# Performance work log

Hardware: AMD Instinct MI355X
Metric: run time of the kernel (lower is better)

Reference implementation:

```python
import jax, jax.numpy as jnp
import numpy as np

E = 8        # num_expert
D = 768      # d_model
H = 3072     # expert hidden = 4*d_model
K = 2        # top_k
N = 4096     # tokens
C = 2048


def setup_inputs() -> dict:
    key = jax.random.key(0)
    k0, k1, k2, k3 = jax.random.split(key, 4)
    moe_inp = jax.random.normal(k0, (N, D), dtype=jnp.float32)
    gate_w = jax.random.normal(k1, (D, E), dtype=jnp.float32) / np.sqrt(D).astype(np.float32)
    gate_b = jnp.zeros((E,), dtype=jnp.float32)
    w1 = jax.random.normal(k2, (E, D, H), dtype=jnp.float32) / np.sqrt(D).astype(np.float32)
    b1 = jnp.zeros((E, H), dtype=jnp.float32)
    w2 = jax.random.normal(k3, (E, H, D), dtype=jnp.float32) / np.sqrt(H).astype(np.float32)
    b2 = jnp.zeros((E, D), dtype=jnp.float32)
    return {"moe_inp": moe_inp, "gate_w": gate_w, "gate_b": gate_b,
            "w1": w1, "b1": b1, "w2": w2, "b2": b2}


def reference(moe_inp, gate_w, gate_b, w1, b1, w2, b2):
    # --- NaiveGate: linear scores, top-k experts, softmax over the k scores ---
    logits = moe_inp @ gate_w + gate_b                      # [N, E]
    top_v, top_i = jax.lax.top_k(logits, K)                 # [N, K]
    gate_score = jax.nn.softmax(top_v, axis=-1)             # [N, K]

    # --- scatter tokens to expert-contiguous capacity buffers (MOEScatter) ---
    flat_e = top_i.reshape(-1)                              # [N*K] expert id per slot
    onehot = jax.nn.one_hot(flat_e, E, dtype=jnp.int32)     # [N*K, E]
    # running position of each token inside its expert's buffer
    pos = jnp.sum(jnp.cumsum(onehot, axis=0) * onehot, axis=1) - 1  # [N*K]
    x_rep = jnp.repeat(moe_inp, K, axis=0)                  # [N*K, D]
    xe = jnp.zeros((E, C, D), dtype=moe_inp.dtype).at[flat_e, pos].set(x_rep, mode='drop')

    # --- grouped expert FFN (expert_fn): per-expert batched GEMMs ---
    h = jax.nn.gelu(jnp.einsum('ecd,edh->ech', xe, w1) + b1[:, None, :])
    ye = jnp.einsum('ech,ehd->ecd', h, w2) + b2[:, None, :]  # [E, C, D]

    # --- gather back to token order (MOEGather) and combine with gate scores ---
    y_flat = ye.at[flat_e, pos].get(mode='fill', fill_value=0.0)  # [N*K, D]
    out = jnp.einsum('nkd,nk->nd', y_flat.reshape(N, K, D), gate_score)
    return out
```

## Files before the change

kernel.cpp:

```cpp
#include <hip/hip_runtime.h>
#include <hip/hip_bf16.h>
#include <math.h>

#define NT    4096
#define DM    768
#define HD    3072
#define NE    8
#define CAP   2048
#define SLOTS_MAX 9216

typedef __attribute__((ext_vector_type(8))) short bf16x8;
typedef __attribute__((ext_vector_type(4))) float f32x4;

__device__ __forceinline__ unsigned short f2bf(float f) {
  unsigned int u = __float_as_uint(f);
  unsigned int r = (u + 0x7fffu + ((u >> 16) & 1u)) >> 16;
  return (unsigned short)r;
}

__device__ __forceinline__ void async16(const unsigned short* g, unsigned short* l) {
  __builtin_amdgcn_global_load_lds((const __attribute__((address_space(1))) void*)g,
                                   (__attribute__((address_space(3))) void*)l,
                                   16, 0, 0);
}

__global__ void convert_x_kernel(const float* __restrict__ x,
                                 unsigned short* __restrict__ xb) {
  int i = (blockIdx.x * 256 + threadIdx.x) * 4;
  float4 v = *(const float4*)(x + i);
  uint2 o;
  o.x = (unsigned int)f2bf(v.x) | ((unsigned int)f2bf(v.y) << 16);
  o.y = (unsigned int)f2bf(v.z) | ((unsigned int)f2bf(v.w) << 16);
  *(uint2*)(xb + i) = o;
}

__global__ void transpose_kernel(const float* __restrict__ src,
                                 unsigned short* __restrict__ dst,
                                 int R, int src_stride, int col_off,
                                 size_t src_e_stride, size_t dst_e_stride) {
  __shared__ unsigned short tile[64][34];
  const float* s = src + blockIdx.z * src_e_stride;
  unsigned short* d = dst + blockIdx.z * dst_e_stride;
  const int r0 = blockIdx.y * 32;
  const int c0 = blockIdx.x * 64;
  const int t = threadIdx.x;
#pragma unroll
  for (int i = 0; i < 4; i++) {
    int row = (t >> 5) + i * 8;
    int cu  = t & 31;
    const float2 v = *(const float2*)(s + (size_t)(r0 + row) * src_stride + col_off + c0 + cu * 2);
    tile[cu * 2][row]     = f2bf(v.x);
    tile[cu * 2 + 1][row] = f2bf(v.y);
  }
  __syncthreads();
#pragma unroll
  for (int i = 0; i < 4; i++) {
    int drow = (t >> 4) + i * 16;
    int ru   = t & 15;
    unsigned int v = *(const unsigned int*)&tile[drow][ru * 2];
    *(unsigned int*)(d + (size_t)(c0 + drow) * R + r0 + ru * 2) = v;
  }
}

__global__ void gate_dots_kernel(const float* __restrict__ inp,
                                 const float* __restrict__ gw,
                                 const float* __restrict__ gb,
                                 int2* __restrict__ tope,
                                 float2* __restrict__ tops) {
  const int tok  = blockIdx.x * 4 + (threadIdx.x >> 6);
  const int lane = threadIdx.x & 63;
  const float* x = inp + (size_t)tok * DM;
  float acc[NE];
#pragma unroll
  for (int e = 0; e < NE; e++) acc[e] = 0.f;
  for (int d = lane; d < DM; d += 64) {
    float xv = x[d];
    const float4 w0 = *(const float4*)(gw + d * NE);
    const float4 w1v = *(const float4*)(gw + d * NE + 4);
    acc[0] += xv * w0.x; acc[1] += xv * w0.y;
    acc[2] += xv * w0.z; acc[3] += xv * w0.w;
    acc[4] += xv * w1v.x; acc[5] += xv * w1v.y;
    acc[6] += xv * w1v.z; acc[7] += xv * w1v.w;
  }
#pragma unroll
  for (int e = 0; e < NE; e++) {
    float v = acc[e];
#pragma unroll
    for (int m = 32; m > 0; m >>= 1) v += __shfl_xor(v, m, 64);
    acc[e] = v + gb[e];
  }
  if (lane == 0) {
    float bv = -1e30f, sv = -1e30f; int bi = 0, si = 0;
#pragma unroll
    for (int e = 0; e < NE; e++) {
      float v = acc[e];
      if (v > bv)      { sv = bv; si = bi; bv = v; bi = e; }
      else if (v > sv) { sv = v;  si = e; }
    }
    float e1 = expf(sv - bv);
    float s0 = 1.f / (1.f + e1);
    float s1 = e1 / (1.f + e1);
    tope[tok] = make_int2(bi, si);
    tops[tok] = make_float2(s0, s1);
  }
}

__device__ __forceinline__ int agg_inc(int* lcnt, int key) {
  const int lane = threadIdx.x & 63;
  int p = 0;
#pragma unroll
  for (int ee = 0; ee < NE; ee++) {
    unsigned long long m = __ballot(key == ee);
    if (m) {
      int leader = __ffsll(m) - 1;
      int n = __popcll(m);
      int b = 0;
      if (lane == leader) b = atomicAdd(&lcnt[ee], n);
      b = __shfl(b, leader, 64);
      if (key == ee) p = b + __popcll(m & ((1ull << lane) - 1ull));
    }
  }
  return p;
}

__global__ void assign_kernel(const int2* __restrict__ tope,
                              int* __restrict__ cnt,
                              int* __restrict__ base,
                              int* __restrict__ src,
                              int2* __restrict__ pos) {
  __shared__ int lcnt[NE];
  const int t = threadIdx.x;
  if (t < NE) lcnt[t] = 0;
  __syncthreads();
  for (int i = t; i < NT; i += 1024) {
    int2 e = tope[i];
    int p0 = agg_inc(lcnt, e.x);
    int p1 = agg_inc(lcnt, e.y);
    if (p0 < CAP) src[e.x * CAP + p0] = i;
    if (p1 < CAP) src[e.y * CAP + p1] = i;
    pos[i] = make_int2(p0, p1);
  }
  __syncthreads();
  if (t == 0) {
    int b = 0;
    for (int e = 0; e < NE; e++) {
      int c = min(lcnt[e], CAP);
      cnt[e] = c;
      base[e] = b;
      b += (c + 127) & ~127;
    }
  }
}

__global__ __launch_bounds__(256) void gemm1_kernel(
    const unsigned short* __restrict__ xb,
    const unsigned short* __restrict__ w1t,
    const float* __restrict__ b1,
    const int* __restrict__ cnt,
    const int* __restrict__ base,
    const int* __restrict__ src,
    unsigned short* __restrict__ h,
    int hoff, int chunk) {
  const int b = blockIdx.x;
  const int e = b & 7;
  const int idx = b >> 3;
  const int m0 = (idx & 15) * 128;
  const int n0 = (idx >> 4) * 128;
  const int count = cnt[e];
  if (m0 >= count) return;
  const int hb = base[e];

  __shared__ unsigned short As[128 * 32];
  __shared__ unsigned short Bs[128 * 32];

  const int t = threadIdx.x;
  const int lane = t & 63;
  const int wave = t >> 6;
  const int r0 = t >> 2;
  const int kc = (t & 3) * 8;

  const int tok0 = (m0 + r0      < count) ? src[e * CAP + m0 + r0]      : 0;
  const int tok1 = (m0 + r0 + 64 < count) ? src[e * CAP + m0 + r0 + 64] : 0;
  const unsigned short* aptr0 = xb + (size_t)tok0 * DM + kc;
  const unsigned short* aptr1 = xb + (size_t)tok1 * DM + kc;
  const unsigned short* w1e = w1t + (size_t)e * chunk * DM;
  const unsigned short* bptr0 = w1e + (size_t)(n0 + r0) * DM + kc;
  const unsigned short* bptr1 = bptr0 + (size_t)64 * DM;

  unsigned short* as0 = As + (wave * 64) * 8;
  unsigned short* as1 = As + (256 + wave * 64) * 8;
  unsigned short* bs0 = Bs + (wave * 64) * 8;
  unsigned short* bs1 = Bs + (256 + wave * 64) * 8;

  const int wrow = (wave >> 1) * 64;
  const int wcol = (wave & 1) * 64;
  const int lrow = lane & 15;
  const int koff = (lane >> 4) * 8;

  f32x4 acc[4][4];
#pragma unroll
  for (int i = 0; i < 4; i++)
#pragma unroll
    for (int j = 0; j < 4; j++) acc[i][j] = (f32x4){0.f, 0.f, 0.f, 0.f};

  for (int k0 = 0; k0 < DM; k0 += 32) {
    async16(aptr0 + k0, as0);
    async16(aptr1 + k0, as1);
    async16(bptr0 + k0, bs0);
    async16(bptr1 + k0, bs1);
    __syncthreads();
    bf16x8 af[4], bfr[4];
#pragma unroll
    for (int i = 0; i < 4; i++)
      af[i] = *(const bf16x8*)(As + (wrow + i * 16 + lrow) * 32 + koff);
#pragma unroll
    for (int j = 0; j < 4; j++)
      bfr[j] = *(const bf16x8*)(Bs + (wcol + j * 16 + lrow) * 32 + koff);
#pragma unroll
    for (int i = 0; i < 4; i++)
#pragma unroll
      for (int j = 0; j < 4; j++)
        acc[i][j] = __builtin_amdgcn_mfma_f32_16x16x32_bf16(af[i], bfr[j], acc[i][j], 0, 0, 0);
    __syncthreads();
  }

  const int q4 = (lane >> 4) * 4;
  const int c = lane & 15;
  unsigned short* hrow = h + (size_t)(hb + m0) * chunk + n0;
#pragma unroll
  for (int j = 0; j < 4; j++) {
    const float bias = b1[e * HD + hoff + n0 + wcol + j * 16 + c];
#pragma unroll
    for (int i = 0; i < 4; i++) {
#pragma unroll
      for (int r = 0; r < 4; r++) {
        int m = wrow + i * 16 + q4 + r;
        float v = acc[i][j][r] + bias;
        float u2 = 1.5957691216f * (v + 0.044715f * v * v * v);
        float g = v / (1.f + __expf(-u2));
        hrow[(size_t)m * chunk + wcol + j * 16 + c] = f2bf(g);
      }
    }
  }
}

__global__ __launch_bounds__(256) void gemm2_kernel(
    const unsigned short* __restrict__ h,
    const unsigned short* __restrict__ w2t,
    const float* __restrict__ b2,
    const int* __restrict__ cnt,
    const int* __restrict__ base,
    float* __restrict__ ye,
    int chunk, int add_b2) {
  const int b = blockIdx.x;
  const int e = b & 7;
  const int idx = b >> 3;
  const int m0 = (idx & 15) * 128;
  const int n0 = (idx >> 4) * 128;
  const int count = cnt[e];
  if (m0 >= count) return;
  const int hb = base[e];

  __shared__ unsigned short As[128 * 32];
  __shared__ unsigned short Bs[128 * 32];

  const int t = threadIdx.x;
  const int lane = t & 63;
  const int wave = t >> 6;
  const int r0 = t >> 2;
  const int kc = (t & 3) * 8;

  const unsigned short* aptr0 = h + (size_t)(hb + m0 + r0) * chunk + kc;
  const unsigned short* aptr1 = aptr0 + (size_t)64 * chunk;
  const unsigned short* w2e = w2t + (size_t)e * DM * chunk;
  const unsigned short* bptr0 = w2e + (size_t)(n0 + r0) * chunk + kc;
  const unsigned short* bptr1 = bptr0 + (size_t)64 * chunk;

  unsigned short* as0 = As + (wave * 64) * 8;
  unsigned short* as1 = As + (256 + wave * 64) * 8;
  unsigned short* bs0 = Bs + (wave * 64) * 8;
  unsigned short* bs1 = Bs + (256 + wave * 64) * 8;

  const int wrow = (wave >> 1) * 64;
  const int wcol = (wave & 1) * 64;
  const int lrow = lane & 15;
  const int koff = (lane >> 4) * 8;

  f32x4 acc[4][4];
#pragma unroll
  for (int i = 0; i < 4; i++)
#pragma unroll
    for (int j = 0; j < 4; j++) acc[i][j] = (f32x4){0.f, 0.f, 0.f, 0.f};

  for (int k0 = 0; k0 < chunk; k0 += 32) {
    async16(aptr0 + k0, as0);
    async16(aptr1 + k0, as1);
    async16(bptr0 + k0, bs0);
    async16(bptr1 + k0, bs1);
    __syncthreads();
    bf16x8 af[4], bfr[4];
#pragma unroll
    for (int i = 0; i < 4; i++)
      af[i] = *(const bf16x8*)(As + (wrow + i * 16 + lrow) * 32 + koff);
#pragma unroll
    for (int j = 0; j < 4; j++)
      bfr[j] = *(const bf16x8*)(Bs + (wcol + j * 16 + lrow) * 32 + koff);
#pragma unroll
    for (int i = 0; i < 4; i++)
#pragma unroll
      for (int j = 0; j < 4; j++)
        acc[i][j] = __builtin_amdgcn_mfma_f32_16x16x32_bf16(af[i], bfr[j], acc[i][j], 0, 0, 0);
    __syncthreads();
  }

  const int q4 = (lane >> 4) * 4;
  const int c = lane & 15;
  float* yrow = ye + (size_t)(hb + m0) * DM + n0;
#pragma unroll
  for (int i = 0; i < 4; i++) {
#pragma unroll
    for (int r = 0; r < 4; r++) {
      int m = wrow + i * 16 + q4 + r;
#pragma unroll
      for (int j = 0; j < 4; j++) {
        int n = wcol + j * 16 + c;
        float v = acc[i][j][r];
        v += add_b2 ? b2[e * DM + n0 + n] : yrow[(size_t)m * DM + n];
        yrow[(size_t)m * DM + n] = v;
      }
    }
  }
}

__global__ void gather_kernel(const float* __restrict__ ye,
                              const int2* __restrict__ tope,
                              const float2* __restrict__ tops,
                              const int2* __restrict__ pos,
                              const int* __restrict__ base,
                              float* __restrict__ out) {
  int idx = blockIdx.x * 256 + threadIdx.x;
  int tok = idx / (DM / 4);
  int d4 = (idx % (DM / 4)) * 4;
  int2 e = tope[tok];
  float2 s = tops[tok];
  int2 p = pos[tok];
  float4 r = make_float4(0.f, 0.f, 0.f, 0.f);
  if (p.x < CAP) {
    const float4 v = *(const float4*)(ye + (size_t)(base[e.x] + p.x) * DM + d4);
    r.x += s.x * v.x; r.y += s.x * v.y; r.z += s.x * v.z; r.w += s.x * v.w;
  }
  if (p.y < CAP) {
    const float4 v = *(const float4*)(ye + (size_t)(base[e.y] + p.y) * DM + d4);
    r.x += s.y * v.x; r.y += s.y * v.y; r.z += s.y * v.z; r.w += s.y * v.w;
  }
  *(float4*)(out + (size_t)tok * DM + d4) = r;
}

extern "C" void kernel_launch(void* const* d_in, const int* in_sizes, int n_in,
                              void* d_out, int out_size, void* d_ws, size_t ws_size,
                              hipStream_t stream) {
  const float* inp = (const float*)d_in[0];
  const float* gw  = (const float*)d_in[1];
  const float* gb  = (const float*)d_in[2];
  const float* w1  = (const float*)d_in[3];
  const float* b1  = (const float*)d_in[4];
  const float* w2  = (const float*)d_in[5];
  const float* b2  = (const float*)d_in[6];
  float* out = (float*)d_out;

  const size_t meta = 164352;
  const int cands[8] = {3072, 1536, 1024, 768, 512, 384, 256, 128};
  int chunk = 128;
  for (int ci = 0; ci < 8; ci++) {
    int c = cands[ci];
    size_t need = meta + (size_t)NT * DM * 2
                + 2 * (size_t)NE * c * DM * 2
                + (size_t)SLOTS_MAX * c * 2
                + (size_t)SLOTS_MAX * DM * 4;
    if (need <= ws_size) { chunk = c; break; }
  }

  char* ws = (char*)d_ws;
  int*    cnt  = (int*)(ws);
  int*    base = (int*)(ws + 256);
  int*    srcb = (int*)(ws + 512);
  int2*   tope = (int2*)(ws + 66048);
  float2* tops = (float2*)(ws + 98816);
  int2*   pos  = (int2*)(ws + 131584);
  size_t off = meta;
  unsigned short* xb = (unsigned short*)(ws + off);   off += (size_t)NT * DM * 2;
  unsigned short* w1tc = (unsigned short*)(ws + off); off += (size_t)NE * chunk * DM * 2;
  unsigned short* w2tc = (unsigned short*)(ws + off); off += (size_t)NE * chunk * DM * 2;
  unsigned short* hc = (unsigned short*)(ws + off);   off += (size_t)SLOTS_MAX * chunk * 2;
  float* ye = (float*)(ws + off);

  convert_x_kernel<<<(NT * DM) / 1024, 256, 0, stream>>>(inp, xb);
  gate_dots_kernel<<<NT / 4, 256, 0, stream>>>(inp, gw, gb, tope, tops);
  assign_kernel<<<1, 1024, 0, stream>>>(tope, cnt, base, srcb, pos);

  for (int c = 0; c < HD; c += chunk) {
    transpose_kernel<<<dim3(chunk / 64, DM / 32, NE), 256, 0, stream>>>(
        w1, w1tc, DM, HD, c, (size_t)DM * HD, (size_t)chunk * DM);
    transpose_kernel<<<dim3(DM / 64, chunk / 32, NE), 256, 0, stream>>>(
        w2 + (size_t)c * DM, w2tc, chunk, DM, 0, (size_t)HD * DM, (size_t)DM * chunk);
    gemm1_kernel<<<NE * 16 * (chunk / 128), 256, 0, stream>>>(
        xb, w1tc, b1, cnt, base, srcb, hc, c, chunk);
    gemm2_kernel<<<NE * 16 * (DM / 128), 256, 0, stream>>>(
        hc, w2tc, b2, cnt, base, ye, chunk, c == 0 ? 1 : 0);
  }

  gather_kernel<<<(NT * DM / 4) / 256, 256, 0, stream>>>(ye, tope, tops, pos, base, out);
}
```

Measured before the change: 397.3 us.

## Split gemm2 K dimension in two and fold b2 bias into gather

The second expert GEMM now splits its reduction dimension into two halves. Each half runs in its own block and writes to its own ye partial buffer, which doubles the grid to improve occupancy. The gather kernel sums the two partials and adds b2, and the w1 and w2 transposed chunks now share one workspace buffer, reordered so gemm1 runs before the w2 transpose. This gives gemm2 more parallelism and may let a larger chunk fit, at the cost of an extra ye buffer, more fp32 writes and gather reads, and a serialization between gemm1 and the w2 transpose.

```diff
diff --git a/kernel.cpp b/kernel.cpp
--- a/kernel.cpp
+++ b/kernel.cpp
@@ -247,19 +247,20 @@
 __global__ __launch_bounds__(256) void gemm2_kernel(
     const unsigned short* __restrict__ h,
     const unsigned short* __restrict__ w2t,
-    const float* __restrict__ b2,
     const int* __restrict__ cnt,
     const int* __restrict__ base,
     float* __restrict__ ye,
-    int chunk, int add_b2) {
+    int chunk, int add_prev) {
   const int b = blockIdx.x;
   const int e = b & 7;
-  const int idx = b >> 3;
+  const int kh = (b >> 3) & 1;
+  const int idx = b >> 4;
   const int m0 = (idx & 15) * 128;
   const int n0 = (idx >> 4) * 128;
   const int count = cnt[e];
   if (m0 >= count) return;
   const int hb = base[e];
+  const int khalf = chunk >> 1;
 
   __shared__ unsigned short As[128 * 32];
   __shared__ unsigned short Bs[128 * 32];
@@ -270,10 +271,10 @@
   const int r0 = t >> 2;
   const int kc = (t & 3) * 8;
 
-  const unsigned short* aptr0 = h + (size_t)(hb + m0 + r0) * chunk + kc;
+  const unsigned short* aptr0 = h + (size_t)(hb + m0 + r0) * chunk + kh * khalf + kc;
   const unsigned short* aptr1 = aptr0 + (size_t)64 * chunk;
   const unsigned short* w2e = w2t + (size_t)e * DM * chunk;
-  const unsigned short* bptr0 = w2e + (size_t)(n0 + r0) * chunk + kc;
+  const unsigned short* bptr0 = w2e + (size_t)(n0 + r0) * chunk + kh * khalf + kc;
   const unsigned short* bptr1 = bptr0 + (size_t)64 * chunk;
 
   unsigned short* as0 = As + (wave * 64) * 8;
@@ -292,7 +293,7 @@
 #pragma unroll
     for (int j = 0; j < 4; j++) acc[i][j] = (f32x4){0.f, 0.f, 0.f, 0.f};
 
-  for (int k0 = 0; k0 < chunk; k0 += 32) {
+  for (int k0 = 0; k0 < khalf; k0 += 32) {
     async16(aptr0 + k0, as0);
     async16(aptr1 + k0, as1);
     async16(bptr0 + k0, bs0);
@@ -315,7 +316,7 @@
 
   const int q4 = (lane >> 4) * 4;
   const int c = lane & 15;
-  float* yrow = ye + (size_t)(hb + m0) * DM + n0;
+  float* yrow = ye + (size_t)kh * SLOTS_MAX * DM + (size_t)(hb + m0) * DM + n0;
 #pragma unroll
   for (int i = 0; i < 4; i++) {
 #pragma unroll
@@ -325,7 +326,7 @@
       for (int j = 0; j < 4; j++) {
         int n = wcol + j * 16 + c;
         float v = acc[i][j][r];
-        v += add_b2 ? b2[e * DM + n0 + n] : yrow[(size_t)m * DM + n];
+        if (add_prev) v += yrow[(size_t)m * DM + n];
         yrow[(size_t)m * DM + n] = v;
       }
     }
@@ -333,6 +334,7 @@
 }
 
 __global__ void gather_kernel(const float* __restrict__ ye,
+                              const float* __restrict__ b2,
                               const int2* __restrict__ tope,
                               const float2* __restrict__ tops,
                               const int2* __restrict__ pos,
@@ -344,14 +346,23 @@
   int2 e = tope[tok];
   float2 s = tops[tok];
   int2 p = pos[tok];
+  const float* ye1 = ye + (size_t)SLOTS_MAX * DM;
   float4 r = make_float4(0.f, 0.f, 0.f, 0.f);
   if (p.x < CAP) {
-    const float4 v = *(const float4*)(ye + (size_t)(base[e.x] + p.x) * DM + d4);
-    r.x += s.x * v.x; r.y += s.x * v.y; r.z += s.x * v.z; r.w += s.x * v.w;
+    size_t row = (size_t)(base[e.x] + p.x) * DM + d4;
+    const float4 va = *(const float4*)(ye + row);
+    const float4 vb = *(const float4*)(ye1 + row);
+    const float4 bb = *(const float4*)(b2 + e.x * DM + d4);
+    r.x += s.x * (va.x + vb.x + bb.x); r.y += s.x * (va.y + vb.y + bb.y);
+    r.z += s.x * (va.z + vb.z + bb.z); r.w += s.x * (va.w + vb.w + bb.w);
   }
   if (p.y < CAP) {
-    const float4 v = *(const float4*)(ye + (size_t)(base[e.y] + p.y) * DM + d4);
-    r.x += s.y * v.x; r.y += s.y * v.y; r.z += s.y * v.z; r.w += s.y * v.w;
+    size_t row = (size_t)(base[e.y] + p.y) * DM + d4;
+    const float4 va = *(const float4*)(ye + row);
+    const float4 vb = *(const float4*)(ye1 + row);
+    const float4 bb = *(const float4*)(b2 + e.y * DM + d4);
+    r.x += s.y * (va.x + vb.x + bb.x); r.y += s.y * (va.y + vb.y + bb.y);
+    r.z += s.y * (va.z + vb.z + bb.z); r.w += s.y * (va.w + vb.w + bb.w);
   }
   *(float4*)(out + (size_t)tok * DM + d4) = r;
 }
@@ -374,9 +385,9 @@
   for (int ci = 0; ci < 8; ci++) {
     int c = cands[ci];
     size_t need = meta + (size_t)NT * DM * 2
-                + 2 * (size_t)NE * c * DM * 2
+                + (size_t)NE * c * DM * 2
                 + (size_t)SLOTS_MAX * c * 2
-                + (size_t)SLOTS_MAX * DM * 4;
+                + 2 * (size_t)SLOTS_MAX * DM * 4;
     if (need <= ws_size) { chunk = c; break; }
   }
 
@@ -388,10 +399,9 @@
   float2* tops = (float2*)(ws + 98816);
   int2*   pos  = (int2*)(ws + 131584);
   size_t off = meta;
-  unsigned short* xb = (unsigned short*)(ws + off);   off += (size_t)NT * DM * 2;
-  unsigned short* w1tc = (unsigned short*)(ws + off); off += (size_t)NE * chunk * DM * 2;
-  unsigned short* w2tc = (unsigned short*)(ws + off); off += (size_t)NE * chunk * DM * 2;
-  unsigned short* hc = (unsigned short*)(ws + off);   off += (size_t)SLOTS_MAX * chunk * 2;
+  unsigned short* xb = (unsigned short*)(ws + off);  off += (size_t)NT * DM * 2;
+  unsigned short* wt = (unsigned short*)(ws + off);  off += (size_t)NE * chunk * DM * 2;
+  unsigned short* hc = (unsigned short*)(ws + off);  off += (size_t)SLOTS_MAX * chunk * 2;
   float* ye = (float*)(ws + off);
 
   convert_x_kernel<<<(NT * DM) / 1024, 256, 0, stream>>>(inp, xb);
@@ -400,14 +410,14 @@
 
   for (int c = 0; c < HD; c += chunk) {
     transpose_kernel<<<dim3(chunk / 64, DM / 32, NE), 256, 0, stream>>>(
-        w1, w1tc, DM, HD, c, (size_t)DM * HD, (size_t)chunk * DM);
+        w1, wt, DM, HD, c, (size_t)DM * HD, (size_t)chunk * DM);
+    gemm1_kernel<<<NE * 16 * (chunk / 128), 256, 0, stream>>>(
+        xb, wt, b1, cnt, base, srcb, hc, c, chunk);
     transpose_kernel<<<dim3(DM / 64, chunk / 32, NE), 256, 0, stream>>>(
-        w2 + (size_t)c * DM, w2tc, chunk, DM, 0, (size_t)HD * DM, (size_t)DM * chunk);
-    gemm1_kernel<<<NE * 16 * (chunk / 128), 256, 0, stream>>>(
-        xb, w1tc, b1, cnt, base, srcb, hc, c, chunk);
-    gemm2_kernel<<<NE * 16 * (DM / 128), 256, 0, stream>>>(
-        hc, w2tc, b2, cnt, base, ye, chunk, c == 0 ? 1 : 0);
-  }
-
-  gather_kernel<<<(NT * DM / 4) / 256, 256, 0, stream>>>(ye, tope, tops, pos, base, out);
-}
+        w2 + (size_t)c * DM, wt, chunk, DM, 0, (size_t)HD * DM, (size_t)DM * chunk);
+    gemm2_kernel<<<NE * 2 * 16 * (DM / 128), 256, 0, stream>>>(
+        hc, wt, cnt, base, ye, chunk, c == 0 ? 0 : 1);
+  }
+
+  gather_kernel<<<(NT * DM / 4) / 256, 256, 0, stream>>>(ye, b2, tope, tops, pos, base, out);
+}
```

New measurement: 382.0 us. 1.04x faster.
